# Kernel optimization log

Hardware: AMD Instinct MI355X
Metric: run time of the kernel (lower is better)

## Reference

```python
import jax, jax.numpy as jnp
import numpy as np

DT = 0.02
TMAX = 3.0
NUM_T = 151  # arange(0, Tmax+dt, dt) -> indices 0..150, 150*dt == Tmax == nonspike
THRESH = 1.0
TIMELINE = jnp.arange(NUM_T, dtype=jnp.float32) * DT          # [T]
TIMELINE_REV = jnp.flip(TIMELINE) + 0.1                        # [T]


def linear_spike_fwd(ti, W):
    """ti: [B, Fin] spike times; W: [Fout, Fin] -> out: [B, Fout] spike times."""
    # ramp: relu(t - ti)  -> [B, Fin, T]
    tmp = jax.nn.relu(TIMELINE[None, None, :] - ti[:, :, None])
    # membrane voltage: mem[b,j,t] = sum_i W[j,i] * tmp[b,i,t]  -> [B, Fout, T]
    mem = jnp.einsum('bit,ji->bjt', tmp, W)
    binary = (mem >= THRESH).astype(jnp.float32)
    binary = binary.at[:, :, -1].set(1.0)  # force spike at last timestep
    # reversed-timeline weighting makes argmax pick the FIRST spike index
    idx = jnp.argmax(binary * TIMELINE_REV, axis=2)
    return idx.astype(jnp.float32) * DT


def setup_inputs() -> dict:
    key = jax.random.key(0)
    k1, k2, k3 = jax.random.split(key, 3)
    B, F0, F1, F2 = 64, 1876, 1024, 10
    ti = jax.random.uniform(k1, (B, F0), dtype=jnp.float32)  # spike times in [0,1)
    W1 = 0.002 + 0.002 * jax.random.normal(k2, (F1, F0), dtype=jnp.float32)
    W2 = 0.001 + 0.001 * jax.random.normal(k3, (F2, F1), dtype=jnp.float32)
    return {"ti": ti, "W1": W1, "W2": W2}


def reference(ti, W1, W2):
    h1 = linear_spike_fwd(ti, W1)
    h2 = linear_spike_fwd(h1, W2)
    return h2
```

## Files before the change

### kernel.cpp

```cpp
#include <hip/hip_runtime.h>
#include <stdint.h>

namespace {

constexpr int   B_    = 64;
constexpr int   F0_   = 1876;
constexpr int   F1_   = 1024;
constexpr int   F2_   = 10;
constexpr int   NT_   = 151;
constexpr float DT_   = 0.02f;
constexpr int   NB1_  = 51;
constexpr int   NSTR_ = 2688;
constexpr int   NGT_  = 336;
constexpr int   GPW_  = 42;
constexpr int   ROWB_ = 4096;
constexpr float SCL_  = 67108864.0f;
constexpr float ISCL_ = 1.0f / 67108864.0f;

constexpr size_t OFF_W1T  = 0;
constexpr size_t OFF_PAIR = 7688192;
constexpr size_t OFF_GB   = OFF_PAIR + 1376256;
constexpr size_t OFF_IDX1 = OFF_GB + 86016;

__global__ __launch_bounds__(256) void k_prep(const float* __restrict__ W1,
                                              const float* __restrict__ ti,
                                              float* __restrict__ W1Tp,
                                              uint2* __restrict__ sPair,
                                              uint32_t* __restrict__ gB) {
  __shared__ uint32_t smem[13184];
  const int t = threadIdx.x;
  if (blockIdx.x < 480) {
    float (*tile)[65] = (float (*)[65])smem;
    const int bx = blockIdx.x;
    const int i0 = (bx % 30) * 64;
    const int j0 = (bx / 30) * 64;
    const int c = t & 63, r4 = t >> 6;
    for (int jj = r4; jj < 64; jj += 4) {
      int i = i0 + c;
      tile[c][jj] = (i < F0_) ? W1[(size_t)(j0 + jj) * F0_ + i] : 0.0f;
    }
    __syncthreads();
    for (int ii = r4; ii < 64; ii += 4) {
      int i = i0 + ii;
      if (i <= F0_) {
        int j = j0 + c;
        int jp = j >> 7, r = j & 127;
        int pc = (jp << 7) + ((r & 63) << 1) + (r >> 6);
        W1Tp[(size_t)i * F1_ + pc] = tile[ii][c];
      }
    }
  } else {
    uint32_t (*hist)[NB1_] = (uint32_t (*)[NB1_])smem;
    uint32_t* pstart = smem + 256 * NB1_;
    uint32_t* cnts   = pstart + 52;
    const int b = blockIdx.x - 480;
    for (int k = 0; k < NB1_; ++k) hist[t][k] = 0;
    __syncthreads();

    const float* tib = ti + (size_t)b * F0_;
    const int n0 = t * 8, n1 = (n0 + 8 < F0_) ? n0 + 8 : F0_;
    for (int n = n0; n < n1; ++n) {
      int k = (int)ceilf(tib[n] * 50.0f);
      k = k < 0 ? 0 : (k > 50 ? 50 : k);
      hist[t][k]++;
    }
    __syncthreads();

    if (t < NB1_) {
      uint32_t run = 0;
      for (int c = 0; c < 256; ++c) { uint32_t x = hist[c][t]; hist[c][t] = run; run += x; }
      cnts[t] = run;
    }
    __syncthreads();
    if (t == 0) {
      uint32_t acc = 0;
      pstart[0] = 0;
      for (int k = 0; k < NB1_; ++k) {
        acc += (cnts[k] + 7u) & ~7u;
        pstart[k + 1] = acc;
      }
    }
    __syncthreads();

    const uint32_t PT = pstart[NB1_];
    uint2*    out = sPair + (size_t)b * NSTR_;
    uint32_t* gb  = gB + (size_t)b * NGT_;
    const uint2 dummy = make_uint2((uint32_t)F0_ * (uint32_t)ROWB_, 0u);

    for (int n = n0; n < n1; ++n) {
      float v = tib[n];
      int k = (int)ceilf(v * 50.0f);
      k = k < 0 ? 0 : (k > 50 ? 50 : k);
      uint32_t pos = pstart[k] + hist[t][k]++;
      out[pos] = make_uint2((uint32_t)n * (uint32_t)ROWB_, __float_as_uint(v));
    }
    if (t < NB1_) {
      uint32_t s0 = pstart[t] + cnts[t], s1 = pstart[t + 1];
      for (uint32_t s = s0; s < s1; ++s) out[s] = dummy;
      for (uint32_t g = pstart[t] >> 3; g < (s1 >> 3); ++g) gb[g] = (uint32_t)t;
    }
    for (uint32_t s = PT + t; s < (uint32_t)NSTR_; s += 256) out[s] = dummy;
    for (uint32_t g = (PT >> 3) + t; g < (uint32_t)NGT_; g += 256) gb[g] = 80u;
  }
}

__global__ __launch_bounds__(512, 4) void k_main1(const uint2* __restrict__ sPair,
                                                  const uint32_t* __restrict__ gB,
                                                  const float* __restrict__ W1Tp,
                                                  uint8_t* __restrict__ idx1) {
  __shared__ uint2    pr[NSTR_];
  __shared__ uint32_t gbw[NGT_];
  __shared__ int binAi[NB1_][128];
  __shared__ int binCi[NB1_][128];
  __shared__ int cand[4][128];
  const int blk  = blockIdx.x;
  const int b    = blk >> 3;
  const int jp   = blk & 7;
  const int tid  = threadIdx.x;
  const int lane = tid & 63;
  const int wv   = __builtin_amdgcn_readfirstlane(tid >> 6);

  {
    const uint4* src = (const uint4*)(sPair + (size_t)b * NSTR_);
    uint4* dst = (uint4*)pr;
    for (int s = tid; s < NSTR_ / 2; s += 512) dst[s] = src[s];
    const uint32_t* gsrc = gB + (size_t)b * NGT_;
    for (int s = tid; s < NGT_; s += 512) gbw[s] = gsrc[s];
    int4* p = (int4*)(&binAi[0][0]);
    for (int s = tid; s < (NB1_ * 128 * 2) / 4; s += 512) p[s] = make_int4(0, 0, 0, 0);
  }
  __syncthreads();

  const char* wb = (const char*)W1Tp;
  const uint32_t col8 = (uint32_t)(jp * 512 + lane * 8);
  const int g0 = wv * GPW_;

  float SA0 = 0.f, SC0 = 0.f, SA1 = 0.f, SC1 = 0.f;
  float SA0p = 0.f, SC0p = 0.f, SA1p = 0.f, SC1p = 0.f;
  uint32_t kcur;

  uint32_t rA[8], rB[8], rC[8], hA, hB, hC;
  float    tA[8], tB[8], tC[8];
  float2   WA[8], WB[8], WC[8];

#define LOADP(S, g) { const int gg = (g) <= (NGT_ - 1) ? (g) : (NGT_ - 1);    \
  _Pragma("unroll") for (int q = 0; q < 4; ++q) {                             \
    uint4 x = *(const uint4*)(&pr[gg * 8 + q * 2]);                           \
    r##S[2 * q]     = x.x; t##S[2 * q]     = __uint_as_float(x.y);            \
    r##S[2 * q + 1] = x.z; t##S[2 * q + 1] = __uint_as_float(x.w); }          \
  h##S = gbw[gg]; }

#define ISSW(S) { _Pragma("unroll") for (int e = 0; e < 8; ++e)               \
    W##S[e] = *(const float2*)(wb + (size_t)(r##S[e] + col8)); }

#define DUMP() { if (kcur < (uint32_t)NB1_) {                                 \
    atomicAdd(&binAi[kcur][lane],      __float2int_rn((SA0 - SA0p) * SCL_));  \
    atomicAdd(&binCi[kcur][lane],      __float2int_rn((SC0 - SC0p) * SCL_));  \
    atomicAdd(&binAi[kcur][64 + lane], __float2int_rn((SA1 - SA1p) * SCL_));  \
    atomicAdd(&binCi[kcur][64 + lane], __float2int_rn((SC1 - SC1p) * SCL_)); }\
  SA0p = SA0; SC0p = SC0; SA1p = SA1; SC1p = SC1; }

#define PROC(S) {                                                             \
  uint32_t kg = __builtin_amdgcn_readfirstlane(h##S);                         \
  if (kg != kcur) { DUMP(); kcur = kg; }                                      \
  _Pragma("unroll") for (int e = 0; e < 8; ++e) {                             \
    SA0 += W##S[e].x; SC0 = fmaf(W##S[e].x, t##S[e], SC0);                    \
    SA1 += W##S[e].y; SC1 = fmaf(W##S[e].y, t##S[e], SC1); } }

  LOADP(A, g0); LOADP(B, g0 + 1);
  ISSW(A); ISSW(B);
  kcur = __builtin_amdgcn_readfirstlane(hA);

#pragma unroll 1
  for (int m = 0; m < GPW_ / 3; ++m) {
    const int g = g0 + 3 * m;
    LOADP(C, g + 2); PROC(A); ISSW(C);
    LOADP(A, g + 3); PROC(B); ISSW(A);
    LOADP(B, g + 4); PROC(C); ISSW(B);
  }
  DUMP();

#undef PROC
#undef DUMP
#undef ISSW
#undef LOADP

  __syncthreads();

  {
    const int jh = wv & 1, tq = wv >> 1;
    const int col = jh * 64 + lane;
    float SA2 = 0.f, SC2 = 0.f;
    int cnd = 151;
    const int t0 = tq * 38;
    const int t1 = (tq == 3) ? NT_ : t0 + 38;
    for (int tt = 0; tt < t1; ++tt) {
      if (tt < NB1_) {
        SA2 += (float)binAi[tt][col] * ISCL_;
        SC2 += (float)binCi[tt][col] * ISCL_;
      }
      if (tt >= t0 && cnd == 151) {
        float m = (float)tt * DT_ * SA2 - SC2;
        if (m >= 1.0f) cnd = tt;
      }
    }
    cand[tq][col] = cnd;
  }
  __syncthreads();
  if (tid < 128) {
    int id = min(min(cand[0][tid], cand[1][tid]),
                 min(cand[2][tid], cand[3][tid]));
    id = min(id, NT_ - 1);
    idx1[((size_t)b << 10) + (jp << 7) + tid] = (uint8_t)id;
  }
}

__global__ __launch_bounds__(256) void k_main2(const uint8_t* __restrict__ idx1,
                                               const float* __restrict__ W2,
                                               float* __restrict__ out) {
  __shared__ float wrow[F1_];
  __shared__ float tirow[F1_];
  __shared__ float part[4][3][64];
  const int blk = blockIdx.x;
  const int b   = blk / 10;
  const int j   = blk - b * 10;
  const int tid = threadIdx.x;
  const int lane = tid & 63, wvv = tid >> 6;

  const float*   w = W2  + (size_t)j * F1_;
  const uint8_t* h = idx1 + (size_t)b * F1_;
  for (int s = tid; s < F1_; s += 256) {
    wrow[s]  = w[s];
    tirow[s] = (float)h[s] * DT_;
  }
  __syncthreads();

  const float tl0 = (float)lane * DT_;
  const float tl1 = (float)(lane + 64) * DT_;
  const float tl2 = (float)(lane + 128) * DT_;
  float m0 = 0.f, m1 = 0.f, m2 = 0.f;
  const int i0 = wvv * 256;
#pragma unroll 4
  for (int i = i0; i < i0 + 256; ++i) {
    float tiv = tirow[i], ww = wrow[i];
    m0 = fmaf(ww, fmaxf(tl0 - tiv, 0.f), m0);
    m1 = fmaf(ww, fmaxf(tl1 - tiv, 0.f), m1);
    m2 = fmaf(ww, fmaxf(tl2 - tiv, 0.f), m2);
  }
  part[wvv][0][lane] = m0;
  part[wvv][1][lane] = m1;
  part[wvv][2][lane] = m2;
  __syncthreads();

  if (wvv == 0) {
    m0 = part[0][0][lane] + part[1][0][lane] + part[2][0][lane] + part[3][0][lane];
    m1 = part[0][1][lane] + part[1][1][lane] + part[2][1][lane] + part[3][1][lane];
    m2 = part[0][2][lane] + part[1][2][lane] + part[2][2][lane] + part[3][2][lane];
    unsigned long long b0 = __ballot(m0 >= 1.0f);
    unsigned long long b1 = __ballot(m1 >= 1.0f);
    unsigned long long b2 = __ballot(m2 >= 1.0f);
    b2 &= (1ull << 23) - 1;
    b2 |= (1ull << 22);
    int tres;
    if (b0)      tres = __ffsll((long long)b0) - 1;
    else if (b1) tres = 64 + __ffsll((long long)b1) - 1;
    else         tres = 128 + __ffsll((long long)b2) - 1;
    if (lane == 0) out[(size_t)b * F2_ + j] = (float)tres * DT_;
  }
}

}

extern "C" void kernel_launch(void* const* d_in, const int* in_sizes, int n_in,
                              void* d_out, int out_size, void* d_ws, size_t ws_size,
                              hipStream_t stream) {
  const float* ti = (const float*)d_in[0];
  const float* W1 = (const float*)d_in[1];
  const float* W2 = (const float*)d_in[2];
  float* out = (float*)d_out;

  char* ws = (char*)d_ws;
  float*    W1Tp = (float*)(ws + OFF_W1T);
  uint2*    sPr  = (uint2*)(ws + OFF_PAIR);
  uint32_t* gBp  = (uint32_t*)(ws + OFF_GB);
  uint8_t*  idx1 = (uint8_t*)(ws + OFF_IDX1);

  hipLaunchKernelGGL(k_prep,  dim3(544), dim3(256), 0, stream, W1, ti, W1Tp, sPr, gBp);
  hipLaunchKernelGGL(k_main1, dim3(512), dim3(512), 0, stream, sPr, gBp, W1Tp, idx1);
  hipLaunchKernelGGL(k_main2, dim3(640), dim3(256), 0, stream, idx1, W2, out);
}
```

Measured before the change: 84.23 us.

## Split main pass into 64-column blocks with dynamic per-batch group counts

Each k_main1 block now covers 64 output columns instead of 128, so the grid doubles to 1024 blocks. Each thread does one scalar W1 load per pair instead of a float2, which removes the interleaved column permutation from W1T. Work per wave now follows the real group count per batch (gNG, written by k_prep), so padding groups are no longer processed. The pipeline shrinks from a 3-stage to a 2-stage software rotation with sched barriers, and occupancy is raised to 6 blocks per CU. The trade-off is that the pair list in shared memory is reloaded by twice as many blocks, and each thread does half the work per memory load.

```diff
diff --git a/kernel.cpp b/kernel.cpp
--- a/kernel.cpp
+++ b/kernel.cpp
@@ -12,7 +12,6 @@
 constexpr int   NB1_  = 51;
 constexpr int   NSTR_ = 2688;
 constexpr int   NGT_  = 336;
-constexpr int   GPW_  = 42;
 constexpr int   ROWB_ = 4096;
 constexpr float SCL_  = 67108864.0f;
 constexpr float ISCL_ = 1.0f / 67108864.0f;
@@ -20,13 +19,15 @@
 constexpr size_t OFF_W1T  = 0;
 constexpr size_t OFF_PAIR = 7688192;
 constexpr size_t OFF_GB   = OFF_PAIR + 1376256;
-constexpr size_t OFF_IDX1 = OFF_GB + 86016;
+constexpr size_t OFF_GNG  = OFF_GB + 86016;
+constexpr size_t OFF_IDX1 = OFF_GNG + 256;
 
 __global__ __launch_bounds__(256) void k_prep(const float* __restrict__ W1,
                                               const float* __restrict__ ti,
-                                              float* __restrict__ W1Tp,
+                                              float* __restrict__ W1T,
                                               uint2* __restrict__ sPair,
-                                              uint32_t* __restrict__ gB) {
+                                              uint32_t* __restrict__ gB,
+                                              uint32_t* __restrict__ gNG) {
   __shared__ uint32_t smem[13184];
   const int t = threadIdx.x;
   if (blockIdx.x < 480) {
@@ -42,12 +43,7 @@
     __syncthreads();
     for (int ii = r4; ii < 64; ii += 4) {
       int i = i0 + ii;
-      if (i <= F0_) {
-        int j = j0 + c;
-        int jp = j >> 7, r = j & 127;
-        int pc = (jp << 7) + ((r & 63) << 1) + (r >> 6);
-        W1Tp[(size_t)i * F1_ + pc] = tile[ii][c];
-      }
+      if (i <= F0_) W1T[(size_t)i * F1_ + j0 + c] = tile[ii][c];
     }
   } else {
     uint32_t (*hist)[NB1_] = (uint32_t (*)[NB1_])smem;
@@ -79,6 +75,7 @@
         acc += (cnts[k] + 7u) & ~7u;
         pstart[k + 1] = acc;
       }
+      gNG[b] = acc >> 3;
     }
     __syncthreads();
 
@@ -104,18 +101,19 @@
   }
 }
 
-__global__ __launch_bounds__(512, 4) void k_main1(const uint2* __restrict__ sPair,
+__global__ __launch_bounds__(512, 6) void k_main1(const uint2* __restrict__ sPair,
                                                   const uint32_t* __restrict__ gB,
-                                                  const float* __restrict__ W1Tp,
+                                                  const uint32_t* __restrict__ gNG,
+                                                  const float* __restrict__ W1T,
                                                   uint8_t* __restrict__ idx1) {
   __shared__ uint2    pr[NSTR_];
   __shared__ uint32_t gbw[NGT_];
-  __shared__ int binAi[NB1_][128];
-  __shared__ int binCi[NB1_][128];
-  __shared__ int cand[4][128];
+  __shared__ int binAi[NB1_][64];
+  __shared__ int binCi[NB1_][64];
+  __shared__ int cand[8][64];
   const int blk  = blockIdx.x;
-  const int b    = blk >> 3;
-  const int jp   = blk & 7;
+  const int b    = blk >> 4;
+  const int jp   = blk & 15;
   const int tid  = threadIdx.x;
   const int lane = tid & 63;
   const int wv   = __builtin_amdgcn_readfirstlane(tid >> 6);
@@ -127,59 +125,65 @@
     const uint32_t* gsrc = gB + (size_t)b * NGT_;
     for (int s = tid; s < NGT_; s += 512) gbw[s] = gsrc[s];
     int4* p = (int4*)(&binAi[0][0]);
-    for (int s = tid; s < (NB1_ * 128 * 2) / 4; s += 512) p[s] = make_int4(0, 0, 0, 0);
-  }
-  __syncthreads();
-
-  const char* wb = (const char*)W1Tp;
-  const uint32_t col8 = (uint32_t)(jp * 512 + lane * 8);
-  const int g0 = wv * GPW_;
-
-  float SA0 = 0.f, SC0 = 0.f, SA1 = 0.f, SC1 = 0.f;
-  float SA0p = 0.f, SC0p = 0.f, SA1p = 0.f, SC1p = 0.f;
+    for (int s = tid; s < (NB1_ * 64 * 2) / 4; s += 512) p[s] = make_int4(0, 0, 0, 0);
+  }
+  __syncthreads();
+
+  const uint32_t NG = gNG[b];
+  const int q  = (int)(NG >> 3), rr = (int)(NG & 7);
+  const int g0  = wv * q + (wv < rr ? wv : rr);
+  const int cnt = q + (wv < rr ? 1 : 0);
+
+  const char* wb = (const char*)W1T;
+  const uint32_t col4 = (uint32_t)((jp << 6) + lane) * 4u;
+
+  float SA = 0.f, SC = 0.f, SAp = 0.f, SCp = 0.f;
   uint32_t kcur;
 
-  uint32_t rA[8], rB[8], rC[8], hA, hB, hC;
-  float    tA[8], tB[8], tC[8];
-  float2   WA[8], WB[8], WC[8];
+  uint32_t rA[8], rB[8], hA, hB;
+  float    tA[8], tB[8];
+  float    WA[8], WB[8];
 
 #define LOADP(S, g) { const int gg = (g) <= (NGT_ - 1) ? (g) : (NGT_ - 1);    \
-  _Pragma("unroll") for (int q = 0; q < 4; ++q) {                             \
-    uint4 x = *(const uint4*)(&pr[gg * 8 + q * 2]);                           \
-    r##S[2 * q]     = x.x; t##S[2 * q]     = __uint_as_float(x.y);            \
-    r##S[2 * q + 1] = x.z; t##S[2 * q + 1] = __uint_as_float(x.w); }          \
+  _Pragma("unroll") for (int q2 = 0; q2 < 4; ++q2) {                          \
+    uint4 x = *(const uint4*)(&pr[gg * 8 + q2 * 2]);                          \
+    r##S[2 * q2]     = x.x; t##S[2 * q2]     = __uint_as_float(x.y);          \
+    r##S[2 * q2 + 1] = x.z; t##S[2 * q2 + 1] = __uint_as_float(x.w); }        \
   h##S = gbw[gg]; }
 
 #define ISSW(S) { _Pragma("unroll") for (int e = 0; e < 8; ++e)               \
-    W##S[e] = *(const float2*)(wb + (size_t)(r##S[e] + col8)); }
+    W##S[e] = *(const float*)(wb + (size_t)(r##S[e] + col4)); }
 
 #define DUMP() { if (kcur < (uint32_t)NB1_) {                                 \
-    atomicAdd(&binAi[kcur][lane],      __float2int_rn((SA0 - SA0p) * SCL_));  \
-    atomicAdd(&binCi[kcur][lane],      __float2int_rn((SC0 - SC0p) * SCL_));  \
-    atomicAdd(&binAi[kcur][64 + lane], __float2int_rn((SA1 - SA1p) * SCL_));  \
-    atomicAdd(&binCi[kcur][64 + lane], __float2int_rn((SC1 - SC1p) * SCL_)); }\
-  SA0p = SA0; SC0p = SC0; SA1p = SA1; SC1p = SC1; }
+    atomicAdd(&binAi[kcur][lane], __float2int_rn((SA - SAp) * SCL_));         \
+    atomicAdd(&binCi[kcur][lane], __float2int_rn((SC - SCp) * SCL_)); }       \
+  SAp = SA; SCp = SC; }
 
 #define PROC(S) {                                                             \
   uint32_t kg = __builtin_amdgcn_readfirstlane(h##S);                         \
   if (kg != kcur) { DUMP(); kcur = kg; }                                      \
   _Pragma("unroll") for (int e = 0; e < 8; ++e) {                             \
-    SA0 += W##S[e].x; SC0 = fmaf(W##S[e].x, t##S[e], SC0);                    \
-    SA1 += W##S[e].y; SC1 = fmaf(W##S[e].y, t##S[e], SC1); } }
-
-  LOADP(A, g0); LOADP(B, g0 + 1);
-  ISSW(A); ISSW(B);
+    SA += W##S[e]; SC = fmaf(W##S[e], t##S[e], SC); } }
+
+#define STEP(Scur, Snxt, g)                                                   \
+  LOADP(Snxt, g); ISSW(Snxt);                                                 \
+  __builtin_amdgcn_sched_barrier(0);                                          \
+  PROC(Scur);
+
+  LOADP(A, g0); ISSW(A);
+  __builtin_amdgcn_sched_barrier(0);
   kcur = __builtin_amdgcn_readfirstlane(hA);
 
+  int m = 0;
 #pragma unroll 1
-  for (int m = 0; m < GPW_ / 3; ++m) {
-    const int g = g0 + 3 * m;
-    LOADP(C, g + 2); PROC(A); ISSW(C);
-    LOADP(A, g + 3); PROC(B); ISSW(A);
-    LOADP(B, g + 4); PROC(C); ISSW(B);
-  }
+  for (; m + 2 <= cnt; m += 2) {
+    STEP(A, B, g0 + m + 1);
+    STEP(B, A, g0 + m + 2);
+  }
+  if (m < cnt) { PROC(A); }
   DUMP();
 
+#undef STEP
 #undef PROC
 #undef DUMP
 #undef ISSW
@@ -188,30 +192,29 @@
   __syncthreads();
 
   {
-    const int jh = wv & 1, tq = wv >> 1;
-    const int col = jh * 64 + lane;
     float SA2 = 0.f, SC2 = 0.f;
     int cnd = 151;
-    const int t0 = tq * 38;
-    const int t1 = (tq == 3) ? NT_ : t0 + 38;
+    const int t0 = wv * 19;
+    const int t1 = (t0 + 19 < NT_) ? t0 + 19 : NT_;
     for (int tt = 0; tt < t1; ++tt) {
       if (tt < NB1_) {
-        SA2 += (float)binAi[tt][col] * ISCL_;
-        SC2 += (float)binCi[tt][col] * ISCL_;
+        SA2 += (float)binAi[tt][lane] * ISCL_;
+        SC2 += (float)binCi[tt][lane] * ISCL_;
       }
       if (tt >= t0 && cnd == 151) {
-        float m = (float)tt * DT_ * SA2 - SC2;
-        if (m >= 1.0f) cnd = tt;
+        float mv = (float)tt * DT_ * SA2 - SC2;
+        if (mv >= 1.0f) cnd = tt;
       }
     }
-    cand[tq][col] = cnd;
-  }
-  __syncthreads();
-  if (tid < 128) {
-    int id = min(min(cand[0][tid], cand[1][tid]),
-                 min(cand[2][tid], cand[3][tid]));
+    cand[wv][lane] = cnd;
+  }
+  __syncthreads();
+  if (tid < 64) {
+    int id = cand[0][tid];
+#pragma unroll
+    for (int w = 1; w < 8; ++w) id = min(id, cand[w][tid]);
     id = min(id, NT_ - 1);
-    idx1[((size_t)b << 10) + (jp << 7) + tid] = (uint8_t)id;
+    idx1[((size_t)b << 10) + (jp << 6) + tid] = (uint8_t)id;
   }
 }
 
@@ -280,12 +283,13 @@
   float* out = (float*)d_out;
 
   char* ws = (char*)d_ws;
-  float*    W1Tp = (float*)(ws + OFF_W1T);
+  float*    W1T  = (float*)(ws + OFF_W1T);
   uint2*    sPr  = (uint2*)(ws + OFF_PAIR);
   uint32_t* gBp  = (uint32_t*)(ws + OFF_GB);
+  uint32_t* gNGp = (uint32_t*)(ws + OFF_GNG);
   uint8_t*  idx1 = (uint8_t*)(ws + OFF_IDX1);
 
-  hipLaunchKernelGGL(k_prep,  dim3(544), dim3(256), 0, stream, W1, ti, W1Tp, sPr, gBp);
-  hipLaunchKernelGGL(k_main1, dim3(512), dim3(512), 0, stream, sPr, gBp, W1Tp, idx1);
-  hipLaunchKernelGGL(k_main2, dim3(640), dim3(256), 0, stream, idx1, W2, out);
-}
+  hipLaunchKernelGGL(k_prep,  dim3(544),  dim3(256), 0, stream, W1, ti, W1T, sPr, gBp, gNGp);
+  hipLaunchKernelGGL(k_main1, dim3(1024), dim3(512), 0, stream, sPr, gBp, gNGp, W1T, idx1);
+  hipLaunchKernelGGL(k_main2, dim3(640),  dim3(256), 0, stream, idx1, W2, out);
+}
```

Measured after the change: 73.88 us. -12.3%, faster.
